# Kernel tuning notes

Hardware: AMD Instinct MI355X
Metric: run time of the kernel (lower is better)

## Reference

```python
import jax, jax.numpy as jnp
import numpy as np
import math

D_MODEL = 1024
N_HEADS = 16
DH = D_MODEL // N_HEADS
THETA = 10000.0


def _rope_tables(S):
    # freqs: (dh/2,)
    inv_freq = 1.0 / (THETA ** (jnp.arange(0, DH, 2, dtype=jnp.float32) / DH))
    ang = jnp.arange(S, dtype=jnp.float32)[:, None] * inv_freq[None, :]  # (S, dh/2)
    cos = jnp.concatenate([jnp.cos(ang), jnp.cos(ang)], axis=-1)  # (S, dh)
    sin = jnp.concatenate([jnp.sin(ang), jnp.sin(ang)], axis=-1)
    return cos, sin


def _apply_rope(x, cos, sin):
    # x: (B, S, H, dh); rotate-half RoPE
    x1, x2 = jnp.split(x, 2, axis=-1)
    rot = jnp.concatenate([-x2, x1], axis=-1)
    c = cos[None, :, None, :]
    s = sin[None, :, None, :]
    return x * c + rot * s


def setup_inputs() -> dict:
    key = jax.random.key(0)
    k1, k2, k3 = jax.random.split(key, 3)
    x = jax.random.normal(k1, (4, 2048, D_MODEL), dtype=jnp.float32)
    qkv = 0.01 * jax.random.normal(k2, (3 * D_MODEL, D_MODEL), dtype=jnp.float32)
    wo = 0.01 * jax.random.normal(k3, (D_MODEL, D_MODEL), dtype=jnp.float32)
    return {"x": x, "qkv": qkv, "wo": wo}


def reference(x, qkv, wo):
    B, S, D = x.shape
    QKV = x @ qkv.T  # (B, S, 3D)
    Q, K, V = jnp.split(QKV, 3, axis=-1)
    q = Q.reshape(B, S, N_HEADS, DH)
    k = K.reshape(B, S, N_HEADS, DH)
    v = V.reshape(B, S, N_HEADS, DH)
    cos, sin = _rope_tables(S)
    q = _apply_rope(q, cos, sin)
    k = _apply_rope(k, cos, sin)
    # (B, H, S, dh)
    q = q.transpose(0, 2, 1, 3)
    k = k.transpose(0, 2, 1, 3)
    v = v.transpose(0, 2, 1, 3)
    scores = jnp.einsum("bhsd,bhtd->bhst", q, k) / math.sqrt(float(DH))
    mask = jnp.tril(jnp.ones((S, S), dtype=scores.dtype))
    scores = scores * mask
    # faithful to original: any exact-zero entry (masked or incidental) -> -inf
    scores = jnp.where(scores == 0.0, -jnp.inf, scores)
    attn = jax.nn.softmax(scores, axis=-1)
    out = jnp.einsum("bhst,bhtd->bhsd", attn, v)  # (B, H, S, dh)
    out = out.transpose(0, 2, 1, 3).reshape(B, S, D)
    return out @ wo.T
```

## Files before the change

kernel.cpp:

```cpp
#include <hip/hip_runtime.h>
#include <math.h>

typedef __bf16 bf16x8 __attribute__((ext_vector_type(8)));
typedef __bf16 bf16x4 __attribute__((ext_vector_type(4)));
typedef float  floatx4 __attribute__((ext_vector_type(4)));
typedef float  floatx2 __attribute__((ext_vector_type(2)));

#define AS1(p) ((__attribute__((address_space(1))) void*)(p))
#define AS3(p) ((__attribute__((address_space(3))) void*)(p))

#define MASKV (-1.0e30f)
#define SOFTMAX_SCALE_LOG2 0.1803368801111244f
#define ROPE_LOG2F 0.4152410118609203f

#define BARRIER do { __builtin_amdgcn_sched_barrier(0); \
                     __builtin_amdgcn_s_barrier(); \
                     __builtin_amdgcn_sched_barrier(0); } while (0)

__global__ __launch_bounds__(256)
void cvt3_kernel(const float* __restrict__ x, const float* __restrict__ qkv,
                 const float* __restrict__ wo, __bf16* __restrict__ xb,
                 __bf16* __restrict__ qkvb, __bf16* __restrict__ wob,
                 float* __restrict__ rt)
{
    const int bi = blockIdx.x;
    if (bi >= 12288) {
        const int e0 = (bi - 12288) * 1024 + threadIdx.x * 4;
#pragma unroll
        for (int j = 0; j < 4; ++j) {
            const int e = e0 + j;
            const int s = e >> 5, d = e & 31;
            const float f = exp2f(-(float)d * ROPE_LOG2F);
            float sn, cs;
            sincosf((float)s * f, &sn, &cs);
            floatx2 t; t[0] = cs; t[1] = sn;
            *(floatx2*)(rt + e * 2) = t;
        }
        return;
    }
    const float* src;
    __bf16* dst;
    int base;
    if (bi < 8192)       { src = x;   dst = xb;   base = bi * 1024; }
    else if (bi < 11264) { src = qkv; dst = qkvb; base = (bi - 8192) * 1024; }
    else                 { src = wo;  dst = wob;  base = (bi - 11264) * 1024; }

    const int i = base + threadIdx.x * 4;
    const floatx4 v = *(const floatx4*)(src + i);
    bf16x4 o;
    o[0] = (__bf16)v[0]; o[1] = (__bf16)v[1];
    o[2] = (__bf16)v[2]; o[3] = (__bf16)v[3];
    *(bf16x4*)(dst + i) = o;
}

__global__ __launch_bounds__(512, 1)
void gemm_rope_kernel(const __bf16* __restrict__ A, const __bf16* __restrict__ BT,
                      __bf16* __restrict__ Qr, __bf16* __restrict__ Kr,
                      __bf16* __restrict__ Vt, const float* __restrict__ rt)
{
    extern __shared__ __align__(16) __bf16 smem[];
    const int id  = blockIdx.x;
    const int xcd = id & 7, lid = id >> 3;
    const int tm  = xcd * 4 + lid / 12;
    const int tn  = lid % 12;
    const int m0  = tm * 256, n0 = tn * 256;

    const int tid  = threadIdx.x;
    const int wave = tid >> 6;
    const int lane = tid & 63;
    const int quad = lane >> 4;
    const int l16  = lane & 15;
    const int wr   = wave >> 2;
    const int wc   = wave & 3;

    const int swz = (l16 & 7) << 4;
    int coff[2];
    coff[0] = (( (quad << 4))     ^ swz) >> 1;
    coff[1] = ((64 | (quad << 4)) ^ swz) >> 1;

    const int aoff = wr * 1024 + l16 * 64;
    const int boff = wc * 2048 + l16 * 64;

    auto stageAH = [&](int bufQ, int h, int k0) {
#pragma unroll
        for (int q = 0; q < 2; ++q) {
            const int o  = (q * 512 + tid) << 4;
            const int lr = o >> 7;
            const int c  = (o & 127) ^ ((lr & 7) << 4);
            const __bf16* src = A + (size_t)(m0 + h * 128 + lr) * 1024 + k0 + (c >> 1);
            __builtin_amdgcn_global_load_lds(AS1(src),
                AS3(smem + bufQ * 32768 + h * 8192 + (q * 8 + wave) * 512), 16, 0, 0);
        }
    };
    auto stageBH = [&](int bufQ, int h, int k0) {
#pragma unroll
        for (int q = 0; q < 2; ++q) {
            const int o  = (q * 512 + tid) << 4;
            const int lr = o >> 7;
            const int c  = (o & 127) ^ ((lr & 7) << 4);
            const int gr = n0 + ((lr >> 4) * 2 + h) * 16 + (lr & 15);
            const __bf16* src = BT + (size_t)gr * 1024 + k0 + (c >> 1);
            __builtin_amdgcn_global_load_lds(AS1(src),
                AS3(smem + bufQ * 32768 + 16384 + h * 8192 + (q * 8 + wave) * 512), 16, 0, 0);
        }
    };

    floatx4 acc[8][4] = {};
    bf16x8 a[4][2], b[4][2];

#define RDA(P, f, ks) (*(const bf16x8*)(smem + (P) * 32768 + ((f) >> 2) * 8192 \
                        + ((f) & 3) * 2048 + aoff + coff[ks]))
#define RDB(P, g, ks) (*(const bf16x8*)(smem + (P) * 32768 + 16384 + ((g) & 1) * 8192 \
                        + ((g) >> 1) * 1024 + boff + coff[ks]))
#define MFQ(FB, G0, G1) do { \
    _Pragma("unroll") for (int fm_ = 0; fm_ < 4; ++fm_) \
    _Pragma("unroll") for (int ks_ = 0; ks_ < 2; ++ks_) { \
        acc[(FB)+fm_][G0] = __builtin_amdgcn_mfma_f32_16x16x32_bf16( \
            a[fm_][ks_], b[G0][ks_], acc[(FB)+fm_][G0], 0, 0, 0); \
        acc[(FB)+fm_][G1] = __builtin_amdgcn_mfma_f32_16x16x32_bf16( \
            a[fm_][ks_], b[G1][ks_], acc[(FB)+fm_][G1], 0, 0, 0); \
    } \
} while (0)

    stageAH(0, 0, 0); stageBH(0, 0, 0); stageBH(0, 1, 0); stageAH(0, 1, 0);
    asm volatile("s_waitcnt vmcnt(4)" ::: "memory");
    BARRIER;

#define GTILE(JT) do { \
    const int P_ = (JT) & 1, Q_ = 1 - P_; \
    const int kn_ = ((JT) + 1) * 64; \
     \
    _Pragma("unroll") for (int fm_ = 0; fm_ < 4; ++fm_) \
    _Pragma("unroll") for (int ks_ = 0; ks_ < 2; ++ks_) a[fm_][ks_] = RDA(P_, fm_, ks_); \
    _Pragma("unroll") for (int ks_ = 0; ks_ < 2; ++ks_) { \
        b[0][ks_] = RDB(P_, 0, ks_); b[2][ks_] = RDB(P_, 2, ks_); } \
    if ((JT) + 1 < 16) { stageAH(Q_, 0, kn_); \
                         asm volatile("s_waitcnt vmcnt(4)" ::: "memory"); } \
    else               { asm volatile("s_waitcnt vmcnt(2)" ::: "memory"); } \
    BARRIER; \
    asm volatile("s_waitcnt lgkmcnt(0)" ::: "memory"); \
    __builtin_amdgcn_s_setprio(1); MFQ(0, 0, 2); __builtin_amdgcn_s_setprio(0); \
     \
    _Pragma("unroll") for (int ks_ = 0; ks_ < 2; ++ks_) { \
        b[1][ks_] = RDB(P_, 1, ks_); b[3][ks_] = RDB(P_, 3, ks_); } \
    if ((JT) + 1 < 16) { stageBH(Q_, 0, kn_); \
                         asm volatile("s_waitcnt vmcnt(4)" ::: "memory"); } \
    else               { asm volatile("s_waitcnt vmcnt(0)" ::: "memory"); } \
    BARRIER; \
    asm volatile("s_waitcnt lgkmcnt(0)" ::: "memory"); \
    __builtin_amdgcn_s_setprio(1); MFQ(0, 1, 3); __builtin_amdgcn_s_setprio(0); \
     \
    _Pragma("unroll") for (int fm_ = 0; fm_ < 4; ++fm_) \
    _Pragma("unroll") for (int ks_ = 0; ks_ < 2; ++ks_) a[fm_][ks_] = RDA(P_, 4 + fm_, ks_); \
    if ((JT) + 1 < 16) stageBH(Q_, 1, kn_); \
    BARRIER; \
    asm volatile("s_waitcnt lgkmcnt(0)" ::: "memory"); \
    __builtin_amdgcn_s_setprio(1); MFQ(4, 1, 3); __builtin_amdgcn_s_setprio(0); \
     \
    if ((JT) + 1 < 16) { stageAH(Q_, 1, kn_); \
                         asm volatile("s_waitcnt vmcnt(4)" ::: "memory"); } \
    BARRIER; \
    __builtin_amdgcn_s_setprio(1); MFQ(4, 0, 2); __builtin_amdgcn_s_setprio(0); \
} while (0)

    GTILE(0);  GTILE(1);  GTILE(2);  GTILE(3);
    GTILE(4);  GTILE(5);  GTILE(6);  GTILE(7);
    GTILE(8);  GTILE(9);  GTILE(10); GTILE(11);
    GTILE(12); GTILE(13); GTILE(14); GTILE(15);

#undef GTILE
#undef MFQ
#undef RDA
#undef RDB

    const int gn0    = n0 + wc * 64;
    const int region = gn0 >> 10;
    const int h      = (gn0 >> 6) & 15;

    if (region == 2) {
#pragma unroll
        for (int f = 0; f < 8; ++f) {
            const int gm = m0 + (f >> 2) * 128 + ((f & 3) * 2 + wr) * 16 + quad * 4;
            const int bb = gm >> 11, s = gm & 2047;
#pragma unroll
            for (int g = 0; g < 4; ++g) {
                const int d = g * 16 + l16;
                bf16x4 w;
#pragma unroll
                for (int r = 0; r < 4; ++r) w[r] = (__bf16)acc[f][g][r];
                *(bf16x4*)(Vt + ((size_t)(bb * 16 + h) * 64 + d) * 2048 + s) = w;
            }
        }
    } else {
        __bf16* dst = region ? Kr : Qr;
        const float sc = region ? 1.0f : SOFTMAX_SCALE_LOG2;
#pragma unroll
        for (int g = 0; g < 2; ++g) {
            const int d1 = g * 16 + l16;
#pragma unroll
            for (int f = 0; f < 8; ++f) {
                const int gm0 = m0 + (f >> 2) * 128 + ((f & 3) * 2 + wr) * 16 + quad * 4;
                const int bb = gm0 >> 11, s0 = gm0 & 2047;
#pragma unroll
                for (int r = 0; r < 4; ++r) {
                    const floatx2 t = *(const floatx2*)(rt + ((s0 + r) * 32 + d1) * 2);
                    const float a1 = acc[f][g][r];
                    const float a2 = acc[f][g + 2][r];
                    __bf16* row = dst + ((size_t)((bb * 16 + h) * 2048 + s0 + r)) * 64;
                    row[d1]      = (__bf16)((a1 * t[0] - a2 * t[1]) * sc);
                    row[d1 + 32] = (__bf16)((a2 * t[0] + a1 * t[1]) * sc);
                }
            }
        }
    }
}

__device__ __forceinline__ void gemm_pipe(const __bf16* __restrict__ Ap,
                                          const __bf16* __restrict__ Bp,
                                          const int m0, const int n0,
                                          __bf16* smem, floatx4 (&acc)[4][4])
{
    const int tid  = threadIdx.x;
    const int wave = tid >> 6;
    const int lane = tid & 63;
    const int quad = lane >> 4;
    const int l16  = lane & 15;
    const int wr   = wave >> 2;
    const int wc   = wave & 3;

    const int arow = wr * 32 + l16;
    const int brow = (wc & 1) * 64 + l16;
    const int bsel = (wc >> 1) * 8192;
    const int swz  = (l16 & 7) << 4;
    int coff[2];
    coff[0] = (( (quad << 4))        ^ swz) >> 1;
    coff[1] = ((64 | (quad << 4))    ^ swz) >> 1;

    auto stageA = [&](int buf, int h, int k0) {
        const int o = tid << 4;
        const int r = o >> 7;
        const int c = (o & 127) ^ ((r & 7) << 4);
        const __bf16* src = Ap + (size_t)(m0 + h * 64 + r) * 1024 + k0 + (c >> 1);
        __builtin_amdgcn_global_load_lds(AS1(src),
            AS3(smem + buf * 24576 + h * 4096 + wave * 512), 16, 0, 0);
    };
    auto stageB = [&](int buf, int h, int k0) {
#pragma unroll
        for (int q = 0; q < 2; ++q) {
            const int o = (q * 512 + tid) << 4;
            const int r = o >> 7;
            const int c = (o & 127) ^ ((r & 7) << 4);
            const __bf16* src = Bp + (size_t)(n0 + h * 128 + r) * 1024 + k0 + (c >> 1);
            __builtin_amdgcn_global_load_lds(AS1(src),
                AS3(smem + buf * 24576 + 8192 + h * 8192 + (q * 8 + wave) * 512), 16, 0, 0);
        }
    };

#define RDA(P, qm, fm, ks) (*(const bf16x8*)(smem + (P) * 24576 + (qm) * 4096 \
                             + ((arow + (fm) * 16) << 6) + coff[ks]))
#define RDB(P, g, ks)      (*(const bf16x8*)(smem + (P) * 24576 + 8192 + bsel \
                             + ((brow + (g) * 16) << 6) + coff[ks]))
#define MFMA16(MB, AH) do { \
    _Pragma("unroll") for (int fm_ = 0; fm_ < 2; ++fm_) \
    _Pragma("unroll") for (int g_ = 0; g_ < 4; ++g_) \
    _Pragma("unroll") for (int ks_ = 0; ks_ < 2; ++ks_) \
        acc[(MB) + fm_][g_] = __builtin_amdgcn_mfma_f32_16x16x32_bf16( \
            AH[fm_][ks_], b[g_][ks_], acc[(MB) + fm_][g_], 0, 0, 0); \
} while (0)

    stageA(0, 0, 0);  stageA(0, 1, 0);  stageB(0, 0, 0);  stageB(0, 1, 0);
    stageA(1, 0, 64); stageA(1, 1, 64); stageB(1, 0, 64); stageB(1, 1, 64);
    asm volatile("s_waitcnt vmcnt(6)" ::: "memory");
    BARRIER;

    bf16x8 a0[2][2], a1[2][2], b[4][2];

#define TILE3(JT) do { \
    const int P_ = (JT) % 3, T_ = ((JT) + 2) % 3; \
    const int kn_ = ((JT) + 2) * 64; \
    _Pragma("unroll") for (int fm_ = 0; fm_ < 2; ++fm_) \
    _Pragma("unroll") for (int ks_ = 0; ks_ < 2; ++ks_) a0[fm_][ks_] = RDA(P_, 0, fm_, ks_); \
    _Pragma("unroll") for (int g_ = 0; g_ < 4; ++g_) \
    _Pragma("unroll") for (int ks_ = 0; ks_ < 2; ++ks_) b[g_][ks_] = RDB(P_, g_, ks_); \
    _Pragma("unroll") for (int fm_ = 0; fm_ < 2; ++fm_) \
    _Pragma("unroll") for (int ks_ = 0; ks_ < 2; ++ks_) a1[fm_][ks_] = RDA(P_, 1, fm_, ks_); \
    if ((JT) + 2 < 16) { stageA(T_, 0, kn_); stageA(T_, 1, kn_); \
                         stageB(T_, 0, kn_); stageB(T_, 1, kn_); } \
    __builtin_amdgcn_s_setprio(1); \
    MFMA16(0, a0); MFMA16(2, a1); \
    __builtin_amdgcn_s_setprio(0); \
    if ((JT) + 2 < 16)      { asm volatile("s_waitcnt vmcnt(6)" ::: "memory"); } \
    else if ((JT) + 1 < 16) { asm volatile("s_waitcnt vmcnt(0)" ::: "memory"); } \
    BARRIER; \
} while (0)

    TILE3(0);  TILE3(1);  TILE3(2);  TILE3(3);
    TILE3(4);  TILE3(5);  TILE3(6);  TILE3(7);
    TILE3(8);  TILE3(9);  TILE3(10); TILE3(11);
    TILE3(12); TILE3(13); TILE3(14); TILE3(15);

#undef TILE3
#undef RDA
#undef RDB
#undef MFMA16
}

__global__ __launch_bounds__(512, 2)
void gemm_bt_kernel(const __bf16* __restrict__ A, const __bf16* __restrict__ BT,
                    float* __restrict__ C)
{
    extern __shared__ __align__(16) __bf16 smem[];
    const int id  = blockIdx.x;
    const int xcd = id & 7, lid = id >> 3;
    const int tm  = xcd * 8 + (lid >> 2);
    const int tn  = lid & 3;
    const int m0  = tm * 128, n0 = tn * 256;

    floatx4 acc[4][4] = {};
    gemm_pipe(A, BT, m0, n0, smem, acc);

    const int tid  = threadIdx.x;
    const int wave = tid >> 6, lane = tid & 63;
    const int quad = lane >> 4, l16 = lane & 15;
    const int wr   = wave >> 2, wc = wave & 3;

#pragma unroll
    for (int f = 0; f < 4; ++f) {
        const int row = m0 + (f >> 1) * 64 + wr * 32 + (f & 1) * 16 + quad * 4;
#pragma unroll
        for (int g = 0; g < 4; ++g) {
            const int col = n0 + wc * 64 + g * 16 + l16;
#pragma unroll
            for (int r = 0; r < 4; ++r)
                C[(size_t)(row + r) * 1024 + col] = acc[f][g][r];
        }
    }
}

__global__ __launch_bounds__(256, 4)
void attn_kernel(const __bf16* __restrict__ Qr, const __bf16* __restrict__ Kr,
                 const __bf16* __restrict__ Vt, __bf16* __restrict__ ctx)
{
    __shared__ __align__(16) __bf16 Ks[64 * 64];
    __shared__ __align__(16) __bf16 Vs[64 * 64];
    __shared__ __align__(16) __bf16 plds[4][16 * 72];

    const int bh   = blockIdx.x;
    const int b    = bh >> 4, h = bh & 15;
    const int tid  = threadIdx.x;
    const int wave = tid >> 6;
    const int lane = tid & 63;
    const int quad = lane >> 4, l16 = lane & 15;
    const int sw   = l16 & 7;

    const __bf16* Qb = Qr + (size_t)bh * 2048 * 64;
    const __bf16* Kb = Kr + (size_t)bh * 2048 * 64;
    const __bf16* Vb = Vt + (size_t)bh * 64 * 2048;
    __bf16* Pw = &plds[wave][0];

    const int row0 = tid >> 3, jg0 = (tid & 7) ^ (row0 & 7);
    const int c1   = 256 + tid;
    const int row1 = c1 >> 3, jg1 = (c1 & 7) ^ (row1 & 7);

    const __bf16* pK0 = Kb + (size_t)row0 * 64 + jg0 * 8;
    const __bf16* pK1 = Kb + (size_t)row1 * 64 + jg1 * 8;
    const __bf16* pV0 = Vb + (size_t)row0 * 2048 + jg0 * 8;
    const __bf16* pV1 = Vb + (size_t)row1 * 2048 + jg1 * 8;

    const int tiles[2] = { (int)blockIdx.y, 31 - (int)blockIdx.y };

    for (int pass = 0; pass < 2; ++pass) {
        const int tq    = tiles[pass];
        const int q0    = tq * 64 + wave * 16;
        const int qa    = q0 + l16;
        const int ntile = tq + 1;

        bf16x8 bq[2];
#pragma unroll
        for (int t = 0; t < 2; ++t)
            bq[t] = *(const bf16x8*)(Qb + (q0 + l16) * 64 + t * 32 + quad * 8);

        floatx4 o[4] = {};
        float lpart = 0.f;

        bf16x8 rk0 = *(const bf16x8*)pK0;
        bf16x8 rk1 = *(const bf16x8*)pK1;
        bf16x8 rv0 = *(const bf16x8*)pV0;
        bf16x8 rv1 = *(const bf16x8*)pV1;

        __syncthreads();

        for (int t = 0; t < ntile; ++t) {
            asm volatile("s_waitcnt vmcnt(0)" ::: "memory");
            *(bf16x8*)(Ks + tid * 8)        = rk0;
            *(bf16x8*)(Ks + 2048 + tid * 8) = rk1;
            *(bf16x8*)(Vs + tid * 8)        = rv0;
            *(bf16x8*)(Vs + 2048 + tid * 8) = rv1;
            asm volatile("s_waitcnt lgkmcnt(0)" ::: "memory");
            BARRIER;

            if (t + 1 < ntile) {
                rk0 = *(const bf16x8*)(pK0 + (size_t)(t + 1) * 4096);
                rk1 = *(const bf16x8*)(pK1 + (size_t)(t + 1) * 4096);
                rv0 = *(const bf16x8*)(pV0 + (t + 1) * 64);
                rv1 = *(const bf16x8*)(pV1 + (t + 1) * 64);
            }

            const int  kt     = t * 64;
            const bool masked = (t == ntile - 1);

            floatx4 s[4] = {};
            __builtin_amdgcn_s_setprio(1);
#pragma unroll
            for (int st = 0; st < 4; ++st) {
                bf16x8 ka0 = *(const bf16x8*)(Ks + (st * 16 + l16) * 64 + ((0 + quad) ^ sw) * 8);
                bf16x8 ka1 = *(const bf16x8*)(Ks + (st * 16 + l16) * 64 + ((4 + quad) ^ sw) * 8);
                s[st] = __builtin_amdgcn_mfma_f32_16x16x32_bf16(ka0, bq[0], s[st], 0, 0, 0);
                s[st] = __builtin_amdgcn_mfma_f32_16x16x32_bf16(ka1, bq[1], s[st], 0, 0, 0);
            }
            __builtin_amdgcn_s_setprio(0);

#pragma unroll
            for (int st = 0; st < 4; ++st) {
                bf16x4 w;
#pragma unroll
                for (int r = 0; r < 4; ++r) {
                    float v = s[st][r];
                    if (masked) {
                        const int key = kt + st * 16 + quad * 4 + r;
                        v = (key > qa) ? MASKV : v;
                    }
                    const float p = __builtin_amdgcn_exp2f(v);
                    lpart += p;
                    w[r] = (__bf16)p;
                }
                *(bf16x4*)(Pw + l16 * 72 + st * 16 + quad * 4) = w;
            }

            asm volatile("s_waitcnt lgkmcnt(0)" ::: "memory");
            bf16x8 ap0 = *(const bf16x8*)(Pw + l16 * 72 + quad * 8);
            bf16x8 ap1 = *(const bf16x8*)(Pw + l16 * 72 + 32 + quad * 8);

            __builtin_amdgcn_s_setprio(1);
#pragma unroll
            for (int nt = 0; nt < 4; ++nt) {
                bf16x8 bv0 = *(const bf16x8*)(Vs + (nt * 16 + l16) * 64 + ((0 + quad) ^ sw) * 8);
                bf16x8 bv1 = *(const bf16x8*)(Vs + (nt * 16 + l16) * 64 + ((4 + quad) ^ sw) * 8);
                o[nt] = __builtin_amdgcn_mfma_f32_16x16x32_bf16(ap0, bv0, o[nt], 0, 0, 0);
                o[nt] = __builtin_amdgcn_mfma_f32_16x16x32_bf16(ap1, bv1, o[nt], 0, 0, 0);
            }
            __builtin_amdgcn_s_setprio(0);

            BARRIER;
        }

        float l = lpart;
        l += __shfl_xor(l, 16, 64);
        l += __shfl_xor(l, 32, 64);
        float lr[4];
#pragma unroll
        for (int r = 0; r < 4; ++r)
            lr[r] = __shfl(l, quad * 4 + r, 64);
#pragma unroll
        for (int nt = 0; nt < 4; ++nt)
#pragma unroll
            for (int r = 0; r < 4; ++r) {
                const int srow = q0 + quad * 4 + r;
                const float inv_l = 1.0f / fmaxf(lr[r], 1e-20f);
                ctx[((size_t)(b * 2048 + srow)) * 1024 + h * 64 + nt * 16 + l16] =
                    (__bf16)(o[nt][r] * inv_l);
            }
    }
}

extern "C" void kernel_launch(void* const* d_in, const int* in_sizes, int n_in,
                              void* d_out, int out_size, void* d_ws, size_t ws_size,
                              hipStream_t stream)
{
    const float* x   = (const float*)d_in[0];
    const float* qkv = (const float*)d_in[1];
    const float* wo  = (const float*)d_in[2];
    float* out = (float*)d_out;

    char* ws = (char*)d_ws;
    const size_t MB = 1024 * 1024;
    __bf16* xb   = (__bf16*)(ws);
    __bf16* qkvb = (__bf16*)(ws + 16 * MB);
    __bf16* wob  = (__bf16*)(ws + 22 * MB);
    __bf16* Qr   = (__bf16*)(ws + 24 * MB);
    __bf16* Kr   = (__bf16*)(ws + 40 * MB);
    __bf16* Vt   = (__bf16*)(ws + 56 * MB);
    __bf16* ctx  = (__bf16*)(ws + 72 * MB);
    float*  rt   = (float*) (ws + 88 * MB);

    hipFuncSetAttribute((const void*)gemm_rope_kernel,
                        hipFuncAttributeMaxDynamicSharedMemorySize, 131072);
    hipFuncSetAttribute((const void*)gemm_bt_kernel,
                        hipFuncAttributeMaxDynamicSharedMemorySize, 147456);

    cvt3_kernel<<<12352, 256, 0, stream>>>(x, qkv, wo, xb, qkvb, wob, rt);
    gemm_rope_kernel<<<384, 512, 131072, stream>>>(xb, qkvb, Qr, Kr, Vt, rt);
    attn_kernel<<<dim3(64, 16), 256, 0, stream>>>(Qr, Kr, Vt, ctx);
    gemm_bt_kernel<<<256, 512, 147456, stream>>>(ctx, wob, out);
}
```

Baseline: 225.4 us.

## Process two adjacent 64-row query tiles per wave to reuse K/V tiles

Each block now handles 128 query rows per pass (two 64-row sub-tiles A and B), so each K/V tile loaded into LDS feeds twice as many MFMAs. The grid is halved and the launch bound's occupancy hint is lowered from 4 to 2. This cuts global K/V traffic and barrier overhead per unit of work. In exchange it raises register pressure and leaves fewer blocks for latency hiding.

```diff
diff --git a/kernel.cpp b/kernel.cpp
--- a/kernel.cpp
+++ b/kernel.cpp
@@ -337,7 +337,7 @@
     }
 }
 
-__global__ __launch_bounds__(256, 4)
+__global__ __launch_bounds__(256, 2)
 void attn_kernel(const __bf16* __restrict__ Qr, const __bf16* __restrict__ Kr,
                  const __bf16* __restrict__ Vt, __bf16* __restrict__ ctx)
 {
@@ -367,21 +367,25 @@
     const __bf16* pV0 = Vb + (size_t)row0 * 2048 + jg0 * 8;
     const __bf16* pV1 = Vb + (size_t)row1 * 2048 + jg1 * 8;
 
-    const int tiles[2] = { (int)blockIdx.y, 31 - (int)blockIdx.y };
+    const int tiles[2] = { (int)blockIdx.y, 15 - (int)blockIdx.y };
 
     for (int pass = 0; pass < 2; ++pass) {
-        const int tq    = tiles[pass];
-        const int q0    = tq * 64 + wave * 16;
-        const int qa    = q0 + l16;
-        const int ntile = tq + 1;
-
-        bf16x8 bq[2];
-#pragma unroll
-        for (int t = 0; t < 2; ++t)
-            bq[t] = *(const bf16x8*)(Qb + (q0 + l16) * 64 + t * 32 + quad * 8);
-
-        floatx4 o[4] = {};
-        float lpart = 0.f;
+        const int sq    = tiles[pass];
+        const int q0A   = sq * 128 + wave * 16;
+        const int q0B   = q0A + 64;
+        const int qaA   = q0A + l16;
+        const int qaB   = q0B + l16;
+        const int ntile = 2 * sq + 2;
+
+        bf16x8 bqA[2], bqB[2];
+#pragma unroll
+        for (int t = 0; t < 2; ++t) {
+            bqA[t] = *(const bf16x8*)(Qb + (q0A + l16) * 64 + t * 32 + quad * 8);
+            bqB[t] = *(const bf16x8*)(Qb + (q0B + l16) * 64 + t * 32 + quad * 8);
+        }
+
+        floatx4 oA[4] = {}, oB[4] = {};
+        float lpA = 0.f, lpB = 0.f;
 
         bf16x8 rk0 = *(const bf16x8*)pK0;
         bf16x8 rk1 = *(const bf16x8*)pK1;
@@ -406,69 +410,109 @@
                 rv1 = *(const bf16x8*)(pV1 + (t + 1) * 64);
             }
 
-            const int  kt     = t * 64;
-            const bool masked = (t == ntile - 1);
-
-            floatx4 s[4] = {};
+            const int  kt      = t * 64;
+            const bool activeA = (t <= 2 * sq);
+            const bool maskA   = (t == 2 * sq);
+            const bool maskB   = (t == ntile - 1);
+
+            floatx4 sA[4] = {}, sB[4] = {};
             __builtin_amdgcn_s_setprio(1);
 #pragma unroll
             for (int st = 0; st < 4; ++st) {
                 bf16x8 ka0 = *(const bf16x8*)(Ks + (st * 16 + l16) * 64 + ((0 + quad) ^ sw) * 8);
                 bf16x8 ka1 = *(const bf16x8*)(Ks + (st * 16 + l16) * 64 + ((4 + quad) ^ sw) * 8);
-                s[st] = __builtin_amdgcn_mfma_f32_16x16x32_bf16(ka0, bq[0], s[st], 0, 0, 0);
-                s[st] = __builtin_amdgcn_mfma_f32_16x16x32_bf16(ka1, bq[1], s[st], 0, 0, 0);
+                sB[st] = __builtin_amdgcn_mfma_f32_16x16x32_bf16(ka0, bqB[0], sB[st], 0, 0, 0);
+                sB[st] = __builtin_amdgcn_mfma_f32_16x16x32_bf16(ka1, bqB[1], sB[st], 0, 0, 0);
+                if (activeA) {
+                    sA[st] = __builtin_amdgcn_mfma_f32_16x16x32_bf16(ka0, bqA[0], sA[st], 0, 0, 0);
+                    sA[st] = __builtin_amdgcn_mfma_f32_16x16x32_bf16(ka1, bqA[1], sA[st], 0, 0, 0);
+                }
             }
             __builtin_amdgcn_s_setprio(0);
+
+            if (activeA) {
+#pragma unroll
+                for (int st = 0; st < 4; ++st) {
+                    bf16x4 w;
+#pragma unroll
+                    for (int r = 0; r < 4; ++r) {
+                        float v = sA[st][r];
+                        if (maskA) {
+                            const int key = kt + st * 16 + quad * 4 + r;
+                            v = (key > qaA) ? MASKV : v;
+                        }
+                        const float p = __builtin_amdgcn_exp2f(v);
+                        lpA += p;
+                        w[r] = (__bf16)p;
+                    }
+                    *(bf16x4*)(Pw + l16 * 72 + st * 16 + quad * 4) = w;
+                }
+                asm volatile("s_waitcnt lgkmcnt(0)" ::: "memory");
+                bf16x8 ap0 = *(const bf16x8*)(Pw + l16 * 72 + quad * 8);
+                bf16x8 ap1 = *(const bf16x8*)(Pw + l16 * 72 + 32 + quad * 8);
+                __builtin_amdgcn_s_setprio(1);
+#pragma unroll
+                for (int nt = 0; nt < 4; ++nt) {
+                    bf16x8 bv0 = *(const bf16x8*)(Vs + (nt * 16 + l16) * 64 + ((0 + quad) ^ sw) * 8);
+                    bf16x8 bv1 = *(const bf16x8*)(Vs + (nt * 16 + l16) * 64 + ((4 + quad) ^ sw) * 8);
+                    oA[nt] = __builtin_amdgcn_mfma_f32_16x16x32_bf16(ap0, bv0, oA[nt], 0, 0, 0);
+                    oA[nt] = __builtin_amdgcn_mfma_f32_16x16x32_bf16(ap1, bv1, oA[nt], 0, 0, 0);
+                }
+                __builtin_amdgcn_s_setprio(0);
+            }
 
 #pragma unroll
             for (int st = 0; st < 4; ++st) {
                 bf16x4 w;
 #pragma unroll
                 for (int r = 0; r < 4; ++r) {
-                    float v = s[st][r];
-                    if (masked) {
+                    float v = sB[st][r];
+                    if (maskB) {
                         const int key = kt + st * 16 + quad * 4 + r;
-                        v = (key > qa) ? MASKV : v;
+                        v = (key > qaB) ? MASKV : v;
                     }
                     const float p = __builtin_amdgcn_exp2f(v);
-                    lpart += p;
+                    lpB += p;
                     w[r] = (__bf16)p;
                 }
                 *(bf16x4*)(Pw + l16 * 72 + st * 16 + quad * 4) = w;
             }
-
             asm volatile("s_waitcnt lgkmcnt(0)" ::: "memory");
-            bf16x8 ap0 = *(const bf16x8*)(Pw + l16 * 72 + quad * 8);
-            bf16x8 ap1 = *(const bf16x8*)(Pw + l16 * 72 + 32 + quad * 8);
-
+            bf16x8 bp0 = *(const bf16x8*)(Pw + l16 * 72 + quad * 8);
+            bf16x8 bp1 = *(const bf16x8*)(Pw + l16 * 72 + 32 + quad * 8);
             __builtin_amdgcn_s_setprio(1);
 #pragma unroll
             for (int nt = 0; nt < 4; ++nt) {
                 bf16x8 bv0 = *(const bf16x8*)(Vs + (nt * 16 + l16) * 64 + ((0 + quad) ^ sw) * 8);
                 bf16x8 bv1 = *(const bf16x8*)(Vs + (nt * 16 + l16) * 64 + ((4 + quad) ^ sw) * 8);
-                o[nt] = __builtin_amdgcn_mfma_f32_16x16x32_bf16(ap0, bv0, o[nt], 0, 0, 0);
-                o[nt] = __builtin_amdgcn_mfma_f32_16x16x32_bf16(ap1, bv1, o[nt], 0, 0, 0);
+                oB[nt] = __builtin_amdgcn_mfma_f32_16x16x32_bf16(bp0, bv0, oB[nt], 0, 0, 0);
+                oB[nt] = __builtin_amdgcn_mfma_f32_16x16x32_bf16(bp1, bv1, oB[nt], 0, 0, 0);
             }
             __builtin_amdgcn_s_setprio(0);
 
             BARRIER;
         }
 
-        float l = lpart;
-        l += __shfl_xor(l, 16, 64);
-        l += __shfl_xor(l, 32, 64);
-        float lr[4];
-#pragma unroll
-        for (int r = 0; r < 4; ++r)
-            lr[r] = __shfl(l, quad * 4 + r, 64);
+        float lA = lpA, lB = lpB;
+        lA += __shfl_xor(lA, 16, 64);  lA += __shfl_xor(lA, 32, 64);
+        lB += __shfl_xor(lB, 16, 64);  lB += __shfl_xor(lB, 32, 64);
+        float lrA[4], lrB[4];
+#pragma unroll
+        for (int r = 0; r < 4; ++r) {
+            lrA[r] = __shfl(lA, quad * 4 + r, 64);
+            lrB[r] = __shfl(lB, quad * 4 + r, 64);
+        }
 #pragma unroll
         for (int nt = 0; nt < 4; ++nt)
 #pragma unroll
             for (int r = 0; r < 4; ++r) {
-                const int srow = q0 + quad * 4 + r;
-                const float inv_l = 1.0f / fmaxf(lr[r], 1e-20f);
-                ctx[((size_t)(b * 2048 + srow)) * 1024 + h * 64 + nt * 16 + l16] =
-                    (__bf16)(o[nt][r] * inv_l);
+                const int   col   = h * 64 + nt * 16 + l16;
+                const int   srowA = q0A + quad * 4 + r;
+                const int   srowB = q0B + quad * 4 + r;
+                ctx[((size_t)(b * 2048 + srowA)) * 1024 + col] =
+                    (__bf16)(oA[nt][r] * (1.0f / fmaxf(lrA[r], 1e-20f)));
+                ctx[((size_t)(b * 2048 + srowB)) * 1024 + col] =
+                    (__bf16)(oB[nt][r] * (1.0f / fmaxf(lrB[r], 1e-20f)));
             }
     }
 }
@@ -500,6 +544,6 @@
 
     cvt3_kernel<<<12352, 256, 0, stream>>>(x, qkv, wo, xb, qkvb, wob, rt);
     gemm_rope_kernel<<<384, 512, 131072, stream>>>(xb, qkvb, Qr, Kr, Vt, rt);
-    attn_kernel<<<dim3(64, 16), 256, 0, stream>>>(Qr, Kr, Vt, ctx);
+    attn_kernel<<<dim3(64, 8), 256, 0, stream>>>(Qr, Kr, Vt, ctx);
     gemm_bt_kernel<<<256, 512, 147456, stream>>>(ctx, wob, out);
 }
```

Measured after the change: 235.4 us. 1.04x slower.
